# Optimization experiments

Measured on AMD Instinct MI355X. Metric: run time of the kernel, lower is better.

Reference implementation:

```python
import jax, jax.numpy as jnp
import numpy as np

B, L, D, H, NL, C = 8, 512, 64, 256, 2, 8
EPS = 1e-5
NEG = -1e9


def _causal_softmax(scores):
    # scores: (B, L, L); lower-triangular causal mask then softmax over last dim
    Ls = scores.shape[-1]
    mask = jnp.tril(jnp.ones((Ls, Ls), dtype=bool))
    return jax.nn.softmax(jnp.where(mask, scores, NEG), axis=-1)


def _attn_plain(x):
    s = jnp.einsum('bld,bmd->blm', x, x)
    return jnp.einsum('blm,bmd->bld', _causal_softmax(s), x)


def _attn_sdpa(x):
    s = jnp.einsum('bld,bmd->blm', x, x) / jnp.sqrt(jnp.float32(x.shape[-1]))
    return jnp.einsum('blm,bmd->bld', _causal_softmax(s), x)


def _attn_additive(x):
    # materializes (B, L, L, D) as in the original module
    s = jnp.tanh(x[:, :, None, :] + x[:, None, :, :]).sum(axis=-1)  # (B,L,L)
    return jnp.einsum('blm,bmd->bld', _causal_softmax(s), x)


def _bn(x, gamma, beta):
    # training-mode BatchNorm1d over (B, L) per feature; x: (B, L, F)
    mu = x.mean(axis=(0, 1))
    var = ((x - mu) ** 2).mean(axis=(0, 1))
    return (x - mu) * jax.lax.rsqrt(var + EPS) * gamma + beta


def _lstm_layer(x, Wih, Whh, bih, bhh):
    # x: (B, L, K) -> (B, L, H). PyTorch gate order: i, f, g, o.
    Hh = Whh.shape[1]
    xg = jnp.einsum('blk,gk->blg', x, Wih) + bih + bhh  # (B, L, 4H)
    xg = jnp.swapaxes(xg, 0, 1)  # (L, B, 4H)

    def step(carry, xt):
        h, c = carry
        g = xt + h @ Whh.T
        i = jax.nn.sigmoid(g[:, 0 * Hh:1 * Hh])
        f = jax.nn.sigmoid(g[:, 1 * Hh:2 * Hh])
        gg = jnp.tanh(g[:, 2 * Hh:3 * Hh])
        o = jax.nn.sigmoid(g[:, 3 * Hh:4 * Hh])
        c = f * c + i * gg
        h = o * jnp.tanh(c)
        return (h, c), h

    h0 = jnp.zeros((x.shape[0], Hh), x.dtype)
    _, hs = jax.lax.scan(step, (h0, h0), xg)
    return jnp.swapaxes(hs, 0, 1)  # (B, L, H)


def setup_inputs() -> dict:
    key = jax.random.key(0)
    ks = jax.random.split(key, 20)
    s = 1.0 / np.sqrt(H)
    u = lambda k, sh: jax.random.uniform(k, sh, jnp.float32, -s, s)
    return {
        'src': jax.random.normal(ks[0], (B, L, D), jnp.float32),
        'attn_w': jax.random.uniform(ks[1], (3, L, D), jnp.float32, 0.5, 1.5),
        'cat_w': jax.random.uniform(ks[2], (3, L, H), jnp.float32, 0.5, 1.5),
        'bn1_gamma': 1.0 + 0.1 * jax.random.normal(ks[3], (3, D), jnp.float32),
        'bn1_beta': 0.1 * jax.random.normal(ks[4], (3, D), jnp.float32),
        'bn2_gamma': 1.0 + 0.1 * jax.random.normal(ks[5], (H,), jnp.float32),
        'bn2_beta': 0.1 * jax.random.normal(ks[6], (H,), jnp.float32),
        'Wih0': u(ks[7], (3, 4 * H, D)),
        'Whh0': u(ks[8], (3, 4 * H, H)),
        'bih0': u(ks[9], (3, 4 * H)),
        'bhh0': u(ks[10], (3, 4 * H)),
        'Wih1': u(ks[11], (3, 4 * H, H)),
        'Whh1': u(ks[12], (3, 4 * H, H)),
        'bih1': u(ks[13], (3, 4 * H)),
        'bhh1': u(ks[14], (3, 4 * H)),
        'fc_W': u(ks[15], (C, H)),
        'fc_b': u(ks[16], (C,)),
    }


def reference(src, attn_w, cat_w, bn1_gamma, bn1_beta, bn2_gamma, bn2_beta,
              Wih0, Whh0, bih0, bhh0, Wih1, Whh1, bih1, bhh1, fc_W, fc_b):
    # three attentions, normalized weighted sum
    outs = jnp.stack([_attn_plain(src), _attn_additive(src), _attn_sdpa(src)])  # (3,B,L,D)
    aw = attn_w / attn_w.sum(axis=0)  # (3, L, D)
    attention_output = jnp.einsum('kbld,kld->bld', outs, aw)

    line1 = _bn(src, bn1_gamma[0], bn1_beta[0])
    line2 = _bn(src + attention_output, bn1_gamma[1], bn1_beta[1])
    line3 = _bn(attention_output, bn1_gamma[2], bn1_beta[2])

    def lstm2(x, i):
        h = _lstm_layer(x, Wih0[i], Whh0[i], bih0[i], bhh0[i])
        return _lstm_layer(h, Wih1[i], Whh1[i], bih1[i], bhh1[i])

    l1 = lstm2(line1, 0)
    l2 = lstm2(line2, 1)
    l3 = lstm2(line3, 2)

    cw = cat_w / cat_w.sum(axis=0)  # (3, L, H)
    cat = l1 * cw[0] + l2 * cw[1] + l3 * cw[2]
    cat = _bn(cat, bn2_gamma, bn2_beta)
    # eval-mode dropout is identity
    return cat[:, -1, :] @ fc_W.T + fc_b  # (B, C)
```

## Files before the change

### kernel.cpp

```cpp
#include <hip/hip_runtime.h>

#define B_ 8
#define L_ 512
#define D_ 64
#define H_ 256
#define GH 1024
#define EPS_ 1e-5f
#define POISON_ 0xAAAAAAAAu

typedef float f32x4 __attribute__((ext_vector_type(4)));
typedef _Float16 half8 __attribute__((ext_vector_type(8)));

__device__ __forceinline__ unsigned short f2h(float f) {
  _Float16 h = (_Float16)f;
  return __builtin_bit_cast(unsigned short, h);
}
__device__ __forceinline__ float h2f(unsigned short s) {
  _Float16 h = __builtin_bit_cast(_Float16, s);
  return (float)h;
}
__device__ __forceinline__ float fast_tanh(float x) {
  return 1.0f - 2.0f / (1.0f + __expf(2.0f * x));
}
__device__ __forceinline__ float fast_sig(float x) {
  return 1.0f / (1.0f + __expf(-x));
}
__device__ __forceinline__ unsigned int load_agent(const unsigned int* p) {
  return __hip_atomic_load(p, __ATOMIC_RELAXED, __HIP_MEMORY_SCOPE_AGENT);
}

__global__ void scores_kernel(const float* __restrict__ src,
                              float* __restrict__ Sp, float* __restrict__ Sa) {
  const int l = blockIdx.x, b = blockIdx.y;
  __shared__ float xl[D_];
  if (threadIdx.x < D_) xl[threadIdx.x] = src[(b * L_ + l) * D_ + threadIdx.x];
  __syncthreads();
  for (int m = threadIdx.x; m <= l; m += blockDim.x) {
    const float4* xr = (const float4*)&src[(b * L_ + m) * D_];
    float dp = 0.f, da = 0.f;
#pragma unroll
    for (int d4 = 0; d4 < D_ / 4; ++d4) {
      float4 v = xr[d4];
      dp += xl[d4*4+0]*v.x + xl[d4*4+1]*v.y + xl[d4*4+2]*v.z + xl[d4*4+3]*v.w;
      da += fast_tanh(xl[d4*4+0]+v.x) + fast_tanh(xl[d4*4+1]+v.y)
          + fast_tanh(xl[d4*4+2]+v.z) + fast_tanh(xl[d4*4+3]+v.w);
    }
    Sp[(b * L_ + l) * L_ + m] = dp;
    Sa[(b * L_ + l) * L_ + m] = da;
  }
}

__global__ void softmax_av_kernel(const float* __restrict__ src, const float* __restrict__ Sp,
                                  const float* __restrict__ Sa, float* __restrict__ outk) {
  const int l = blockIdx.x, b = blockIdx.y, k = blockIdx.z;
  const int lane = threadIdx.x;
  __shared__ float p[L_];
  const float* row = (k == 1) ? &Sa[(b * L_ + l) * L_] : &Sp[(b * L_ + l) * L_];
  const float scale = (k == 2) ? 0.125f : 1.0f;
  float mx = -1e30f;
  for (int m = lane; m <= l; m += 64) { float v = row[m] * scale; p[m] = v; mx = fmaxf(mx, v); }
#pragma unroll
  for (int off = 32; off > 0; off >>= 1) mx = fmaxf(mx, __shfl_xor(mx, off, 64));
  float sum = 0.f;
  for (int m = lane; m <= l; m += 64) { float e = __expf(p[m] - mx); p[m] = e; sum += e; }
#pragma unroll
  for (int off = 32; off > 0; off >>= 1) sum += __shfl_xor(sum, off, 64);
  __syncthreads();
  const float inv = 1.0f / sum;
  float acc = 0.f;
  for (int m = 0; m <= l; ++m) acc += p[m] * src[(b * L_ + m) * D_ + lane];
  outk[((k * B_ + b) * L_ + l) * D_ + lane] = acc * inv;
}

__global__ void combine_kernel(const float* __restrict__ outk, const float* __restrict__ attn_w,
                               float* __restrict__ attn) {
  int i = blockIdx.x * blockDim.x + threadIdx.x;
  if (i >= B_ * L_ * D_) return;
  int ld = i & (L_ * D_ - 1);
  float w0 = attn_w[ld], w1 = attn_w[L_ * D_ + ld], w2 = attn_w[2 * L_ * D_ + ld];
  float o0 = outk[i], o1 = outk[B_ * L_ * D_ + i], o2 = outk[2 * B_ * L_ * D_ + i];
  attn[i] = (o0 * w0 + o1 * w1 + o2 * w2) / (w0 + w1 + w2);
}

__global__ void bn1_kernel(const float* __restrict__ src, const float* __restrict__ attn,
                           const float* __restrict__ gamma, const float* __restrict__ beta,
                           float* __restrict__ line_in) {
  const int d = blockIdx.x, line = blockIdx.y;
  float s1 = 0.f, s2 = 0.f;
  for (int i = threadIdx.x; i < B_ * L_; i += blockDim.x) {
    float v = (line == 0) ? src[i * D_ + d]
            : (line == 1) ? src[i * D_ + d] + attn[i * D_ + d]
                          : attn[i * D_ + d];
    s1 += v; s2 += v * v;
  }
#pragma unroll
  for (int off = 32; off > 0; off >>= 1) { s1 += __shfl_xor(s1, off, 64); s2 += __shfl_xor(s2, off, 64); }
  __shared__ float a1[4], a2[4];
  __shared__ float mean_s, rstd_s;
  int w = threadIdx.x >> 6;
  if ((threadIdx.x & 63) == 0) { a1[w] = s1; a2[w] = s2; }
  __syncthreads();
  if (threadIdx.x == 0) {
    float t1 = a1[0] + a1[1] + a1[2] + a1[3];
    float t2 = a2[0] + a2[1] + a2[2] + a2[3];
    float mean = t1 / (float)(B_ * L_);
    float var = t2 / (float)(B_ * L_) - mean * mean;
    mean_s = mean; rstd_s = rsqrtf(var + EPS_);
  }
  __syncthreads();
  const float mean = mean_s;
  const float gs = gamma[line * D_ + d] * rstd_s, be = beta[line * D_ + d];
  for (int i = threadIdx.x; i < B_ * L_; i += blockDim.x) {
    float v = (line == 0) ? src[i * D_ + d]
            : (line == 1) ? src[i * D_ + d] + attn[i * D_ + d]
                          : attn[i * D_ + d];
    line_in[line * B_ * L_ * D_ + i * D_ + d] = (v - mean) * gs + be;
  }
}

template <int IN_K>
__device__ __forceinline__ void rec_body(
    const float* __restrict__ in_f32,
    const unsigned short* __restrict__ in_b16,
    const float* __restrict__ Wih, const float* __restrict__ Whh,
    const float* __restrict__ bih, const float* __restrict__ bhh,
    unsigned short* __restrict__ hseq,
    int line, int s,
    unsigned short* hprev, unsigned short* inbuf,
    float (*gbuf)[32][8], float (*biasS)[32]) {
  constexpr int INROW = IN_K + 8;
  constexpr int NKT_IN = IN_K / 32;
  const int tid = threadIdx.x, w = tid >> 6, lane = tid & 63;
  const int q = lane >> 4, col = lane & 15;

  half8 whhF[2][8];
  half8 wihF[2][NKT_IN];
#pragma unroll
  for (int T = 0; T < 2; ++T) {
    const int n = w * H_ + s * 32 + T * 16 + col;
    const float* wr = &Whh[(line * GH + n) * H_];
#pragma unroll
    for (int kt = 0; kt < 8; ++kt) {
      const float* pk = wr + kt * 32 + q * 8;
      half8 t;
#pragma unroll
      for (int j = 0; j < 8; ++j) t[j] = (_Float16)pk[j];
      whhF[T][kt] = t;
    }
    const float* wr2 = &Wih[(line * GH + n) * IN_K];
#pragma unroll
    for (int kt = 0; kt < NKT_IN; ++kt) {
      const float* pk = wr2 + kt * 32 + q * 8;
      half8 t;
#pragma unroll
      for (int j = 0; j < 8; ++j) t[j] = (_Float16)pk[j];
      wihF[T][kt] = t;
    }
  }
  if (tid < 128) {
    int g = tid >> 5, j = tid & 31;
    int n = g * H_ + s * 32 + j;
    biasS[g][j] = bih[line * GH + n] + bhh[line * GH + n];
  }
  for (int i = tid; i < 16 * 264; i += 256) hprev[i] = 0;
  for (int i = tid; i < 16 * INROW; i += 256) inbuf[i] = 0;

  int gdst[4];
  bool gremote[4];
  int goff[4];
#pragma unroll
  for (int rr = 0; rr < 4; ++rr) {
    int u = tid + rr * 256;
    int r = u >> 7, v = u & 127, b = v >> 4, pz = v & 15;
    int cidx = r * 32 + pz * 2;
    gremote[rr] = (r != s);
    gdst[rr] = b * 264 + cidx;
    goff[rr] = b * H_ + cidx;
  }

  if constexpr (IN_K == 64) {
#pragma unroll
    for (int r = 0; r < 2; ++r) {
      int idx = tid + r * 256;
      int b = idx >> 6, d = idx & 63;
      inbuf[b * INROW + d] = f2h(in_f32[(line * B_ * L_ + b * L_ + 0) * D_ + d]);
    }
  } else {
    const unsigned int* sa[4];
    unsigned int sv[4];
#pragma unroll
    for (int r = 0; r < 4; ++r) {
      int u = tid + r * 256;
      int b = u >> 7, pr = u & 127;
      sa[r] = (const unsigned int*)&in_b16[((line * L_ + 0) * B_ + b) * H_ + pr * 2];
    }
    bool ready = false;
    while (!ready) {
#pragma unroll
      for (int r = 0; r < 4; ++r) sv[r] = load_agent(sa[r]);
      ready = true;
#pragma unroll
      for (int r = 0; r < 4; ++r) ready = ready && (sv[r] != POISON_);
    }
#pragma unroll
    for (int r = 0; r < 4; ++r) {
      int u = tid + r * 256;
      int b = u >> 7, pr = u & 127;
      *(unsigned int*)&inbuf[b * INROW + pr * 2] = sv[r];
    }
  }

  float c0 = 0.f, c1 = 0.f;
  const int ub = tid & 7, jp = (tid >> 3) * 2;
  __syncthreads();

  for (int t = 0; t < L_; ++t) {
    f32x4 acc0 = {0.f, 0.f, 0.f, 0.f}, acc1 = {0.f, 0.f, 0.f, 0.f};
#pragma unroll
    for (int kt = 0; kt < NKT_IN; ++kt) {
      half8 a = *(const half8*)&inbuf[col * INROW + kt * 32 + q * 8];
      acc0 = __builtin_amdgcn_mfma_f32_16x16x32_f16(a, wihF[0][kt], acc0, 0, 0, 0);
      acc1 = __builtin_amdgcn_mfma_f32_16x16x32_f16(a, wihF[1][kt], acc1, 0, 0, 0);
    }
#pragma unroll
    for (int kt = 0; kt < 8; ++kt) {
      half8 a = *(const half8*)&hprev[col * 264 + kt * 32 + q * 8];
      acc0 = __builtin_amdgcn_mfma_f32_16x16x32_f16(a, whhF[0][kt], acc0, 0, 0, 0);
      acc1 = __builtin_amdgcn_mfma_f32_16x16x32_f16(a, whhF[1][kt], acc1, 0, 0, 0);
    }
    if (q < 2) {
#pragma unroll
      for (int r = 0; r < 4; ++r) {
        gbuf[w][col][q * 4 + r] = acc0[r];
        gbuf[w][16 + col][q * 4 + r] = acc1[r];
      }
    }
    __syncthreads();

    if (tid < 128) {
      float gi0 = gbuf[0][jp][ub] + biasS[0][jp];
      float gf0 = gbuf[1][jp][ub] + biasS[1][jp];
      float gg0 = gbuf[2][jp][ub] + biasS[2][jp];
      float go0 = gbuf[3][jp][ub] + biasS[3][jp];
      float gi1 = gbuf[0][jp+1][ub] + biasS[0][jp+1];
      float gf1 = gbuf[1][jp+1][ub] + biasS[1][jp+1];
      float gg1 = gbuf[2][jp+1][ub] + biasS[2][jp+1];
      float go1 = gbuf[3][jp+1][ub] + biasS[3][jp+1];
      c0 = fast_sig(gf0) * c0 + fast_sig(gi0) * fast_tanh(gg0);
      c1 = fast_sig(gf1) * c1 + fast_sig(gi1) * fast_tanh(gg1);
      float h0 = fast_sig(go0) * fast_tanh(c0);
      float h1 = fast_sig(go1) * fast_tanh(c1);
      unsigned int packed = (unsigned int)f2h(h0) | ((unsigned int)f2h(h1) << 16);
      if (packed == POISON_) packed ^= 1u;
      __hip_atomic_store(
          (unsigned int*)&hseq[((line * L_ + t) * B_ + ub) * H_ + s * 32 + jp],
          packed, __ATOMIC_RELAXED, __HIP_MEMORY_SCOPE_AGENT);
      *(unsigned int*)&hprev[ub * 264 + s * 32 + jp] = packed;
    }

    if (t == L_ - 1) break;

    const unsigned short* hrow = &hseq[(size_t)(line * L_ + t) * B_ * H_];
    const unsigned int* ga[4];
    unsigned int gv[4];
#pragma unroll
    for (int rr = 0; rr < 4; ++rr) ga[rr] = (const unsigned int*)(hrow + goff[rr]);

    if constexpr (IN_K == 64) {
#pragma unroll
      for (int r = 0; r < 2; ++r) {
        int idx = tid + r * 256;
        int b = idx >> 6, d = idx & 63;
        inbuf[b * INROW + d] = f2h(in_f32[(line * B_ * L_ + b * L_ + t + 1) * D_ + d]);
      }
      bool ready = false;
      while (!ready) {
#pragma unroll
        for (int rr = 0; rr < 4; ++rr) gv[rr] = load_agent(ga[rr]);
        ready = true;
#pragma unroll
        for (int rr = 0; rr < 4; ++rr)
          ready = ready && (!gremote[rr] || gv[rr] != POISON_);
      }
    } else {
      const unsigned int* sa[4];
      unsigned int sv[4];
#pragma unroll
      for (int r = 0; r < 4; ++r) {
        int u = tid + r * 256;
        int b = u >> 7, pr = u & 127;
        sa[r] = (const unsigned int*)&in_b16[((line * L_ + t + 1) * B_ + b) * H_ + pr * 2];
      }
      bool ready = false;
      while (!ready) {
#pragma unroll
        for (int rr = 0; rr < 4; ++rr) gv[rr] = load_agent(ga[rr]);
#pragma unroll
        for (int r = 0; r < 4; ++r) sv[r] = load_agent(sa[r]);
        ready = true;
#pragma unroll
        for (int rr = 0; rr < 4; ++rr)
          ready = ready && (!gremote[rr] || gv[rr] != POISON_);
#pragma unroll
        for (int r = 0; r < 4; ++r) ready = ready && (sv[r] != POISON_);
      }
#pragma unroll
      for (int r = 0; r < 4; ++r) {
        int u = tid + r * 256;
        int b = u >> 7, pr = u & 127;
        *(unsigned int*)&inbuf[b * INROW + pr * 2] = sv[r];
      }
    }
#pragma unroll
    for (int rr = 0; rr < 4; ++rr)
      if (gremote[rr]) *(unsigned int*)&hprev[gdst[rr]] = gv[rr];
    __syncthreads();
  }
}

__global__ __launch_bounds__(256, 1) void rec_fused_kernel(
    const float* __restrict__ line_in,
    const float* __restrict__ Wih0, const float* __restrict__ Whh0,
    const float* __restrict__ bih0, const float* __restrict__ bhh0,
    const float* __restrict__ Wih1, const float* __restrict__ Whh1,
    const float* __restrict__ bih1, const float* __restrict__ bhh1,
    unsigned short* __restrict__ hseq0, unsigned short* __restrict__ hseq1) {
  __shared__ unsigned short hprev[16 * 264];
  __shared__ unsigned short inbuf[16 * 264];
  __shared__ float gbuf[4][32][8];
  __shared__ float biasS[4][32];
  const int blk = blockIdx.x;
  const int layer = blk / 24, rem = blk % 24;
  const int line = rem >> 3, s = rem & 7;
  if (layer == 0)
    rec_body<64>(line_in, nullptr, Wih0, Whh0, bih0, bhh0, hseq0,
                 line, s, hprev, inbuf, gbuf, biasS);
  else
    rec_body<256>(nullptr, hseq0, Wih1, Whh1, bih1, bhh1, hseq1,
                  line, s, hprev, inbuf, gbuf, biasS);
}

__global__ void bn2stats_kernel(const unsigned short* __restrict__ hseq1,
                                const float* __restrict__ cat_w, float* __restrict__ stats) {
  const int h = blockIdx.x;
  float s1 = 0.f, s2 = 0.f;
  for (int i = threadIdx.x; i < B_ * L_; i += blockDim.x) {
    int l = i >> 3, b = i & 7;
    float w0 = cat_w[(0 * L_ + l) * H_ + h], w1 = cat_w[(1 * L_ + l) * H_ + h],
          w2 = cat_w[(2 * L_ + l) * H_ + h];
    float v0 = h2f(hseq1[((0 * L_ + l) * B_ + b) * H_ + h]);
    float v1 = h2f(hseq1[((1 * L_ + l) * B_ + b) * H_ + h]);
    float v2 = h2f(hseq1[((2 * L_ + l) * B_ + b) * H_ + h]);
    float v = (v0 * w0 + v1 * w1 + v2 * w2) / (w0 + w1 + w2);
    s1 += v; s2 += v * v;
  }
#pragma unroll
  for (int off = 32; off > 0; off >>= 1) { s1 += __shfl_xor(s1, off, 64); s2 += __shfl_xor(s2, off, 64); }
  __shared__ float a1[4], a2[4];
  int w = threadIdx.x >> 6;
  if ((threadIdx.x & 63) == 0) { a1[w] = s1; a2[w] = s2; }
  __syncthreads();
  if (threadIdx.x == 0) {
    float t1 = a1[0] + a1[1] + a1[2] + a1[3];
    float t2 = a2[0] + a2[1] + a2[2] + a2[3];
    float mean = t1 / (float)(B_ * L_);
    float var = t2 / (float)(B_ * L_) - mean * mean;
    stats[2 * h] = mean;
    stats[2 * h + 1] = rsqrtf(var + EPS_);
  }
}

__global__ void final_kernel(const unsigned short* __restrict__ hseq1,
                             const float* __restrict__ cat_w, const float* __restrict__ stats,
                             const float* __restrict__ gamma, const float* __restrict__ beta,
                             const float* __restrict__ fcW, const float* __restrict__ fcb,
                             float* __restrict__ out) {
  const int h = threadIdx.x;
  __shared__ float vmat[B_][H_];
  const float mean = stats[2 * h], rstd = stats[2 * h + 1];
  const float g = gamma[h], be = beta[h];
  const int l = L_ - 1;
  float w0 = cat_w[(0 * L_ + l) * H_ + h], w1 = cat_w[(1 * L_ + l) * H_ + h],
        w2 = cat_w[(2 * L_ + l) * H_ + h];
  const float wsum = w0 + w1 + w2;
  for (int b = 0; b < B_; ++b) {
    float v0 = h2f(hseq1[((0 * L_ + l) * B_ + b) * H_ + h]);
    float v1 = h2f(hseq1[((1 * L_ + l) * B_ + b) * H_ + h]);
    float v2 = h2f(hseq1[((2 * L_ + l) * B_ + b) * H_ + h]);
    float v = (v0 * w0 + v1 * w1 + v2 * w2) / wsum;
    vmat[b][h] = (v - mean) * rstd * g + be;
  }
  __syncthreads();
  if (h < 64) {
    int b = h >> 3, c = h & 7;
    float acc = fcb[c];
    for (int k = 0; k < H_; ++k) acc += vmat[b][k] * fcW[c * H_ + k];
    out[b * 8 + c] = acc;
  }
}

extern "C" void kernel_launch(void* const* d_in, const int* in_sizes, int n_in,
                              void* d_out, int out_size, void* d_ws, size_t ws_size,
                              hipStream_t stream) {
  (void)in_sizes; (void)n_in; (void)out_size; (void)ws_size;
  const float* src       = (const float*)d_in[0];
  const float* attn_w    = (const float*)d_in[1];
  const float* cat_w     = (const float*)d_in[2];
  const float* bn1_gamma = (const float*)d_in[3];
  const float* bn1_beta  = (const float*)d_in[4];
  const float* bn2_gamma = (const float*)d_in[5];
  const float* bn2_beta  = (const float*)d_in[6];
  const float* Wih0      = (const float*)d_in[7];
  const float* Whh0      = (const float*)d_in[8];
  const float* bih0      = (const float*)d_in[9];
  const float* bhh0      = (const float*)d_in[10];
  const float* Wih1      = (const float*)d_in[11];
  const float* Whh1      = (const float*)d_in[12];
  const float* bih1      = (const float*)d_in[13];
  const float* bhh1      = (const float*)d_in[14];
  const float* fcW       = (const float*)d_in[15];
  const float* fcb       = (const float*)d_in[16];
  float* out = (float*)d_out;

  char* p = (char*)d_ws;
  float* Sp = (float*)p;                      p += (size_t)B_ * L_ * L_ * 4;
  float* Sa = (float*)p;                      p += (size_t)B_ * L_ * L_ * 4;
  float* outk = (float*)p;                    p += (size_t)3 * B_ * L_ * D_ * 4;
  float* attn = (float*)p;                    p += (size_t)B_ * L_ * D_ * 4;
  float* line_in = (float*)p;                 p += (size_t)3 * B_ * L_ * D_ * 4;
  float* stats = (float*)p;                   p += (size_t)512 * 4;
  unsigned short* hseq0 = (unsigned short*)p; p += (size_t)3 * L_ * B_ * H_ * 2;
  unsigned short* hseq1 = (unsigned short*)p; p += (size_t)3 * L_ * B_ * H_ * 2;

  scores_kernel<<<dim3(L_, B_), dim3(256), 0, stream>>>(src, Sp, Sa);
  softmax_av_kernel<<<dim3(L_, B_, 3), dim3(64), 0, stream>>>(src, Sp, Sa, outk);
  combine_kernel<<<dim3((B_ * L_ * D_) / 256), dim3(256), 0, stream>>>(outk, attn_w, attn);
  bn1_kernel<<<dim3(D_, 3), dim3(256), 0, stream>>>(src, attn, bn1_gamma, bn1_beta, line_in);
  rec_fused_kernel<<<dim3(48), dim3(256), 0, stream>>>(
      line_in, Wih0, Whh0, bih0, bhh0, Wih1, Whh1, bih1, bhh1, hseq0, hseq1);
  bn2stats_kernel<<<dim3(H_), dim3(256), 0, stream>>>(hseq1, cat_w, stats);
  final_kernel<<<dim3(1), dim3(256), 0, stream>>>(hseq1, cat_w, stats, bn2_gamma, bn2_beta,
                                                  fcW, fcb, out);
}
```

Before: 1.300 ms.

## Restructure LSTM: one block per recurrence, precompute input projections in separate GEMMs

Replaces the 8-block-per-line recurrence, which exchanged hidden-state slices through global memory every step, with a single 512-thread block per line and layer that keeps the full Whh in registers and LDS. The input projections move out of the serial loop: layer 0's into a separate xg0 kernel, layer 1's into concurrent GEMM blocks that consume hseq0 in chunks through poison-flag polling. This targets per-step cross-block synchronisation latency and the input-projection work on the critical path. The cost is extra workspace for the fp16 xg buffers, a large dynamic LDS allocation, and reliance on all 18 blocks being co-resident for the flag-based producer/consumer handoff.

```diff
diff --git a/kernel.cpp b/kernel.cpp
--- a/kernel.cpp
+++ b/kernel.cpp
@@ -10,6 +10,9 @@
 
 typedef float f32x4 __attribute__((ext_vector_type(4)));
 typedef _Float16 half8 __attribute__((ext_vector_type(8)));
+typedef unsigned long long u64_;
+
+#define MFMA16(a, b, c) __builtin_amdgcn_mfma_f32_16x16x32_f16((a), (b), (c), 0, 0, 0)
 
 __device__ __forceinline__ unsigned short f2h(float f) {
   _Float16 h = (_Float16)f;
@@ -25,8 +28,18 @@
 __device__ __forceinline__ float fast_sig(float x) {
   return 1.0f / (1.0f + __expf(-x));
 }
-__device__ __forceinline__ unsigned int load_agent(const unsigned int* p) {
-  return __hip_atomic_load(p, __ATOMIC_RELAXED, __HIP_MEMORY_SCOPE_AGENT);
+__device__ __forceinline__ unsigned int pack2h(float x, float y) {
+  return (unsigned int)f2h(x) | ((unsigned int)f2h(y) << 16);
+}
+__device__ __forceinline__ unsigned int fixp(unsigned int d) { return d == POISON_ ? (d ^ 1u) : d; }
+__device__ __forceinline__ u64_ fixp64(u64_ v) {
+  return (u64_)fixp((unsigned int)v) | ((u64_)fixp((unsigned int)(v >> 32)) << 32);
+}
+__device__ __forceinline__ u64_ ldA64(const void* p) {
+  return __hip_atomic_load((const u64_*)p, __ATOMIC_RELAXED, __HIP_MEMORY_SCOPE_AGENT);
+}
+__device__ __forceinline__ void stA64(void* p, u64_ v) {
+  __hip_atomic_store((u64_*)p, v, __ATOMIC_RELAXED, __HIP_MEMORY_SCOPE_AGENT);
 }
 
 __global__ void scores_kernel(const float* __restrict__ src,
@@ -118,226 +131,263 @@
   }
 }
 
-template <int IN_K>
-__device__ __forceinline__ void rec_body(
-    const float* __restrict__ in_f32,
-    const unsigned short* __restrict__ in_b16,
-    const float* __restrict__ Wih, const float* __restrict__ Whh,
-    const float* __restrict__ bih, const float* __restrict__ bhh,
-    unsigned short* __restrict__ hseq,
-    int line, int s,
-    unsigned short* hprev, unsigned short* inbuf,
-    float (*gbuf)[32][8], float (*biasS)[32]) {
-  constexpr int INROW = IN_K + 8;
-  constexpr int NKT_IN = IN_K / 32;
-  const int tid = threadIdx.x, w = tid >> 6, lane = tid & 63;
-  const int q = lane >> 4, col = lane & 15;
-
-  half8 whhF[2][8];
-  half8 wihF[2][NKT_IN];
-#pragma unroll
-  for (int T = 0; T < 2; ++T) {
-    const int n = w * H_ + s * 32 + T * 16 + col;
-    const float* wr = &Whh[(line * GH + n) * H_];
-#pragma unroll
-    for (int kt = 0; kt < 8; ++kt) {
-      const float* pk = wr + kt * 32 + q * 8;
-      half8 t;
-#pragma unroll
-      for (int j = 0; j < 8; ++j) t[j] = (_Float16)pk[j];
-      whhF[T][kt] = t;
-    }
-    const float* wr2 = &Wih[(line * GH + n) * IN_K];
-#pragma unroll
-    for (int kt = 0; kt < NKT_IN; ++kt) {
-      const float* pk = wr2 + kt * 32 + q * 8;
-      half8 t;
-#pragma unroll
-      for (int j = 0; j < 8; ++j) t[j] = (_Float16)pk[j];
-      wihF[T][kt] = t;
-    }
-  }
-  if (tid < 128) {
-    int g = tid >> 5, j = tid & 31;
-    int n = g * H_ + s * 32 + j;
-    biasS[g][j] = bih[line * GH + n] + bhh[line * GH + n];
-  }
-  for (int i = tid; i < 16 * 264; i += 256) hprev[i] = 0;
-  for (int i = tid; i < 16 * INROW; i += 256) inbuf[i] = 0;
-
-  int gdst[4];
-  bool gremote[4];
-  int goff[4];
-#pragma unroll
-  for (int rr = 0; rr < 4; ++rr) {
-    int u = tid + rr * 256;
-    int r = u >> 7, v = u & 127, b = v >> 4, pz = v & 15;
-    int cidx = r * 32 + pz * 2;
-    gremote[rr] = (r != s);
-    gdst[rr] = b * 264 + cidx;
-    goff[rr] = b * H_ + cidx;
-  }
-
-  if constexpr (IN_K == 64) {
-#pragma unroll
-    for (int r = 0; r < 2; ++r) {
-      int idx = tid + r * 256;
-      int b = idx >> 6, d = idx & 63;
-      inbuf[b * INROW + d] = f2h(in_f32[(line * B_ * L_ + b * L_ + 0) * D_ + d]);
-    }
+__global__ __launch_bounds__(512) void xg0_kernel(
+    const float* __restrict__ line_in, const float* __restrict__ Wih0,
+    const float* __restrict__ bih0, const float* __restrict__ bhh0,
+    unsigned short* __restrict__ xg0) {
+  __shared__ unsigned short af[256][72];
+  const int tc = blockIdx.x, line = blockIdx.y;
+  const int tid = threadIdx.x;
+  for (int idx = tid; idx < 4096; idx += 512) {
+    int row = idx >> 4, d4 = (idx & 15) * 4;
+    int t = tc * 32 + (row >> 3), b = row & 7;
+    float4 v = *(const float4*)&line_in[(size_t)line * (B_ * L_ * D_) + ((size_t)b * L_ + t) * D_ + d4];
+    u64_ pk = (u64_)f2h(v.x) | ((u64_)f2h(v.y) << 16) | ((u64_)f2h(v.z) << 32) | ((u64_)f2h(v.w) << 48);
+    *(u64_*)&af[row][d4] = pk;
+  }
+  __syncthreads();
+  const int lane = tid & 63, w = tid >> 6, col = lane & 15, q = lane >> 4;
+  unsigned short* xg_l = xg0 + (size_t)line * 4194304;
+#pragma unroll 1
+  for (int nt = w; nt < 64; nt += 8) {
+    const int n = nt * 16 + col;
+    const float* wr = &Wih0[((size_t)line * GH + n) * D_ + q * 8];
+    half8 b0, b1;
+    {
+      float4 u0 = *(const float4*)wr, u1 = *(const float4*)(wr + 4);
+      float4 u2 = *(const float4*)(wr + 32), u3 = *(const float4*)(wr + 36);
+      b0[0] = (_Float16)u0.x; b0[1] = (_Float16)u0.y; b0[2] = (_Float16)u0.z; b0[3] = (_Float16)u0.w;
+      b0[4] = (_Float16)u1.x; b0[5] = (_Float16)u1.y; b0[6] = (_Float16)u1.z; b0[7] = (_Float16)u1.w;
+      b1[0] = (_Float16)u2.x; b1[1] = (_Float16)u2.y; b1[2] = (_Float16)u2.z; b1[3] = (_Float16)u2.w;
+      b1[4] = (_Float16)u3.x; b1[5] = (_Float16)u3.y; b1[6] = (_Float16)u3.z; b1[7] = (_Float16)u3.w;
+    }
+    const float bias = bih0[line * GH + n] + bhh0[line * GH + n];
+#pragma unroll 1
+    for (int mt = 0; mt < 16; ++mt) {
+      f32x4 acc = {0.f, 0.f, 0.f, 0.f};
+      half8 av0 = *(const half8*)&af[mt * 16 + col][q * 8];
+      half8 av1 = *(const half8*)&af[mt * 16 + col][32 + q * 8];
+      acc = MFMA16(av0, b0, acc);
+      acc = MFMA16(av1, b1, acc);
+      unsigned int d0 = fixp(pack2h(acc[0] + bias, acc[1] + bias));
+      unsigned int d1 = fixp(pack2h(acc[2] + bias, acc[3] + bias));
+      int t = tc * 32 + mt * 2 + (q >> 1);
+      *(u64_*)&xg_l[(size_t)t * 8192 + n * 8 + (q & 1) * 4] = (u64_)d0 | ((u64_)d1 << 32);
+    }
+  }
+}
+
+__device__ __forceinline__ void rec_core(
+    const float* __restrict__ Whh_l, const unsigned short* __restrict__ xg_l,
+    unsigned short* __restrict__ hseq_l, unsigned short* sm) {
+  unsigned short* wlds = sm;
+  unsigned short* hb = sm + 65536;
+  const int tid = threadIdx.x, lane = tid & 63, w = tid >> 6;
+  const int col = lane & 15, q = lane >> 4, qq = q & 1;
+
+  for (int idx = tid; idx < 8192; idx += 512) {
+    int rec = idx >> 6, l = idx & 63;
+    int ww = rec >> 4, tau = (rec >> 1) & 7, ktp = rec & 1;
+    int n = (tau >> 1) * 256 + ww * 32 + (tau & 1) * 16 + (l & 15);
+    const float* p = &Whh_l[(size_t)n * H_ + 192 + ktp * 32 + (l >> 4) * 8];
+    float4 u0 = *(const float4*)p, u1 = *(const float4*)(p + 4);
+    half8 tf;
+    tf[0] = (_Float16)u0.x; tf[1] = (_Float16)u0.y; tf[2] = (_Float16)u0.z; tf[3] = (_Float16)u0.w;
+    tf[4] = (_Float16)u1.x; tf[5] = (_Float16)u1.y; tf[6] = (_Float16)u1.z; tf[7] = (_Float16)u1.w;
+    *(half8*)&wlds[(size_t)idx * 8] = tf;
+  }
+
+  half8 wf[6][8];
+#pragma unroll
+  for (int g = 0; g < 4; ++g)
+#pragma unroll
+    for (int h2 = 0; h2 < 2; ++h2) {
+      const float* wr = &Whh_l[(size_t)(g * 256 + w * 32 + h2 * 16 + col) * H_];
+#pragma unroll
+      for (int kt = 0; kt < 6; ++kt) {
+        const float* p = wr + kt * 32 + q * 8;
+        float4 u0 = *(const float4*)p, u1 = *(const float4*)(p + 4);
+        half8 tf;
+        tf[0] = (_Float16)u0.x; tf[1] = (_Float16)u0.y; tf[2] = (_Float16)u0.z; tf[3] = (_Float16)u0.w;
+        tf[4] = (_Float16)u1.x; tf[5] = (_Float16)u1.y; tf[6] = (_Float16)u1.z; tf[7] = (_Float16)u1.w;
+        wf[kt][g * 2 + h2] = tf;
+      }
+    }
+
+  for (int i = tid; i < 8448; i += 512) hb[i] = 0;
+  float c_[2][4] = {{0.f, 0.f, 0.f, 0.f}, {0.f, 0.f, 0.f, 0.f}};
+  __syncthreads();
+
+  int cur = 0;
+#pragma unroll 1
+  for (int t = 0; t < L_; ++t) {
+    const unsigned short* hbr = hb + cur * 4224;
+    unsigned short* hbw = hb + (cur ^ 1) * 4224;
+
+    if (t > 0) {
+      u64_ v = fixp64(*(const u64_*)&hbr[w * 264 + lane * 4]);
+      stA64(&hseq_l[((size_t)(t - 1) * 8 + w) * 256 + lane * 4], v);
+    }
+
+#pragma unroll
+    for (int h2 = 0; h2 < 2; ++h2) {
+      u64_ xv[4];
+      const size_t xb = (size_t)t * 8192 + (size_t)qq * 4;
+#pragma unroll
+      for (int g = 0; g < 4; ++g)
+        xv[g] = ldA64(&xg_l[xb + (unsigned)(g * 2048 + w * 256 + h2 * 128 + col * 8)]);
+
+      f32x4 a0 = {0.f, 0.f, 0.f, 0.f}, a1 = a0, a2 = a0, a3 = a0;
+#pragma unroll
+      for (int kt = 0; kt < 6; ++kt) {
+        half8 av = *(const half8*)&hbr[col * 264 + kt * 32 + q * 8];
+        a0 = MFMA16(av, wf[kt][0 + h2], a0);
+        a1 = MFMA16(av, wf[kt][2 + h2], a1);
+        a2 = MFMA16(av, wf[kt][4 + h2], a2);
+        a3 = MFMA16(av, wf[kt][6 + h2], a3);
+      }
+#pragma unroll
+      for (int ktp = 0; ktp < 2; ++ktp) {
+        half8 av = *(const half8*)&hbr[col * 264 + 192 + ktp * 32 + q * 8];
+        half8 b0 = *(const half8*)&wlds[((w * 16 + (0 + h2) * 2 + ktp) * 64 + lane) * 8];
+        half8 b1 = *(const half8*)&wlds[((w * 16 + (2 + h2) * 2 + ktp) * 64 + lane) * 8];
+        half8 b2 = *(const half8*)&wlds[((w * 16 + (4 + h2) * 2 + ktp) * 64 + lane) * 8];
+        half8 b3 = *(const half8*)&wlds[((w * 16 + (6 + h2) * 2 + ktp) * 64 + lane) * 8];
+        a0 = MFMA16(av, b0, a0); a1 = MFMA16(av, b1, a1);
+        a2 = MFMA16(av, b2, a2); a3 = MFMA16(av, b3, a3);
+      }
+
+      for (;;) {
+        bool bad = false;
+#pragma unroll
+        for (int g = 0; g < 4; ++g)
+          bad = bad | ((unsigned int)xv[g] == POISON_) | ((unsigned int)(xv[g] >> 32) == POISON_);
+        if (!bad) break;
+#pragma unroll
+        for (int g = 0; g < 4; ++g)
+          xv[g] = ldA64(&xg_l[xb + (unsigned)(g * 2048 + w * 256 + h2 * 128 + col * 8)]);
+      }
+
+      if (lane < 32) {
+#pragma unroll
+        for (int rr = 0; rr < 4; ++rr) {
+          float gi = a0[rr] + h2f((unsigned short)(xv[0] >> (16 * rr)));
+          float gf = a1[rr] + h2f((unsigned short)(xv[1] >> (16 * rr)));
+          float gg = a2[rr] + h2f((unsigned short)(xv[2] >> (16 * rr)));
+          float go = a3[rr] + h2f((unsigned short)(xv[3] >> (16 * rr)));
+          float cv = fast_sig(gf) * c_[h2][rr] + fast_sig(gi) * fast_tanh(gg);
+          c_[h2][rr] = cv;
+          float hv = fast_sig(go) * fast_tanh(cv);
+          hbw[(q * 4 + rr) * 264 + w * 32 + h2 * 16 + col] = f2h(hv);
+        }
+      }
+    }
+    __syncthreads();
+    cur ^= 1;
+  }
+  {
+    const unsigned short* hbr = hb + cur * 4224;
+    u64_ v = fixp64(*(const u64_*)&hbr[w * 264 + lane * 4]);
+    stA64(&hseq_l[((size_t)(L_ - 1) * 8 + w) * 256 + lane * 4], v);
+  }
+}
+
+__device__ __forceinline__ void gemm1_core(
+    const unsigned short* __restrict__ hs0_l, const float* __restrict__ Wih_l,
+    const float* __restrict__ bih_l, const float* __restrict__ bhh_l,
+    unsigned short* __restrict__ xg_l, int nq, unsigned short* sm) {
+  unsigned short* wlds = sm;
+  unsigned short* as_ = sm + 65536;
+  const int tid = threadIdx.x, lane = tid & 63, w = tid >> 6;
+  const int col = lane & 15, q = lane >> 4;
+
+  for (int idx = tid; idx < 8192; idx += 512) {
+    int rec = idx >> 6, l = idx & 63;
+    int nt = rec >> 3, kt = rec & 7;
+    int n = nq * 256 + nt * 16 + (l & 15);
+    const float* p = &Wih_l[(size_t)n * H_ + kt * 32 + (l >> 4) * 8];
+    float4 u0 = *(const float4*)p, u1 = *(const float4*)(p + 4);
+    half8 tf;
+    tf[0] = (_Float16)u0.x; tf[1] = (_Float16)u0.y; tf[2] = (_Float16)u0.z; tf[3] = (_Float16)u0.w;
+    tf[4] = (_Float16)u1.x; tf[5] = (_Float16)u1.y; tf[6] = (_Float16)u1.z; tf[7] = (_Float16)u1.w;
+    *(half8*)&wlds[(size_t)idx * 8] = tf;
+  }
+  const int nA = nq * 256 + w * 16 + col, nB = nA + 128;
+  const float biasA = bih_l[nA] + bhh_l[nA];
+  const float biasB = bih_l[nB] + bhh_l[nB];
+  __syncthreads();
+
+#pragma unroll 1
+  for (int c = 0; c < 128; ++c) {
+    const u64_* src = (const u64_*)&hs0_l[(size_t)c * 8192] + tid * 4;
+    u64_ v0, v1, v2, v3;
+    for (;;) {
+      v0 = ldA64(src + 0); v1 = ldA64(src + 1); v2 = ldA64(src + 2); v3 = ldA64(src + 3);
+      bool bad = ((unsigned int)v0 == POISON_) | ((unsigned int)(v0 >> 32) == POISON_)
+               | ((unsigned int)v1 == POISON_) | ((unsigned int)(v1 >> 32) == POISON_)
+               | ((unsigned int)v2 == POISON_) | ((unsigned int)(v2 >> 32) == POISON_)
+               | ((unsigned int)v3 == POISON_) | ((unsigned int)(v3 >> 32) == POISON_);
+      if (!bad) break;
+    }
+    __syncthreads();
+    {
+      u64_* d = (u64_*)&as_[(tid >> 4) * 264 + (tid & 15) * 16];
+      d[0] = v0; d[1] = v1; d[2] = v2; d[3] = v3;
+    }
+    __syncthreads();
+
+    half8 afr[2][8];
+#pragma unroll
+    for (int mt = 0; mt < 2; ++mt)
+#pragma unroll
+      for (int kt = 0; kt < 8; ++kt)
+        afr[mt][kt] = *(const half8*)&as_[(mt * 16 + col) * 264 + kt * 32 + q * 8];
+
+    const int t0 = c * 4;
+#pragma unroll
+    for (int half = 0; half < 2; ++half) {
+      const int nt = w + half * 8;
+      const float bias = half ? biasB : biasA;
+      f32x4 c0 = {0.f, 0.f, 0.f, 0.f}, c1 = c0;
+#pragma unroll
+      for (int kt = 0; kt < 8; ++kt) {
+        half8 bf = *(const half8*)&wlds[((nt * 8 + kt) * 64 + lane) * 8];
+        c0 = MFMA16(afr[0][kt], bf, c0);
+        c1 = MFMA16(afr[1][kt], bf, c1);
+      }
+      const int n = nq * 256 + nt * 16 + col;
+#pragma unroll
+      for (int mt = 0; mt < 2; ++mt) {
+        const f32x4 A = mt ? c1 : c0;
+        unsigned int d0 = fixp(pack2h(A[0] + bias, A[1] + bias));
+        unsigned int d1 = fixp(pack2h(A[2] + bias, A[3] + bias));
+        int t = t0 + mt * 2 + (q >> 1);
+        stA64(&xg_l[(size_t)t * 8192 + n * 8 + (q & 1) * 4], (u64_)d0 | ((u64_)d1 << 32));
+      }
+    }
+  }
+}
+
+__global__ __launch_bounds__(512, 2) void rec2_kernel(
+    const float* __restrict__ Whh0, const float* __restrict__ Whh1,
+    const float* __restrict__ Wih1, const float* __restrict__ bih1,
+    const float* __restrict__ bhh1,
+    const unsigned short* __restrict__ xg0, unsigned short* __restrict__ xg1,
+    unsigned short* __restrict__ hseq0, unsigned short* __restrict__ hseq1) {
+  extern __shared__ unsigned short sm[];
+  const int blk = blockIdx.x;
+  if (blk < 6) {
+    const int line = blk % 3, layer = blk / 3;
+    const float* Whh_l = (layer ? Whh1 : Whh0) + (size_t)line * GH * H_;
+    const unsigned short* xg_l = (layer ? (const unsigned short*)xg1 : xg0) + (size_t)line * 4194304;
+    unsigned short* hs_l = (layer ? hseq1 : hseq0) + (size_t)line * (L_ * B_ * H_);
+    rec_core(Whh_l, xg_l, hs_l, sm);
   } else {
-    const unsigned int* sa[4];
-    unsigned int sv[4];
-#pragma unroll
-    for (int r = 0; r < 4; ++r) {
-      int u = tid + r * 256;
-      int b = u >> 7, pr = u & 127;
-      sa[r] = (const unsigned int*)&in_b16[((line * L_ + 0) * B_ + b) * H_ + pr * 2];
-    }
-    bool ready = false;
-    while (!ready) {
-#pragma unroll
-      for (int r = 0; r < 4; ++r) sv[r] = load_agent(sa[r]);
-      ready = true;
-#pragma unroll
-      for (int r = 0; r < 4; ++r) ready = ready && (sv[r] != POISON_);
-    }
-#pragma unroll
-    for (int r = 0; r < 4; ++r) {
-      int u = tid + r * 256;
-      int b = u >> 7, pr = u & 127;
-      *(unsigned int*)&inbuf[b * INROW + pr * 2] = sv[r];
-    }
-  }
-
-  float c0 = 0.f, c1 = 0.f;
-  const int ub = tid & 7, jp = (tid >> 3) * 2;
-  __syncthreads();
-
-  for (int t = 0; t < L_; ++t) {
-    f32x4 acc0 = {0.f, 0.f, 0.f, 0.f}, acc1 = {0.f, 0.f, 0.f, 0.f};
-#pragma unroll
-    for (int kt = 0; kt < NKT_IN; ++kt) {
-      half8 a = *(const half8*)&inbuf[col * INROW + kt * 32 + q * 8];
-      acc0 = __builtin_amdgcn_mfma_f32_16x16x32_f16(a, wihF[0][kt], acc0, 0, 0, 0);
-      acc1 = __builtin_amdgcn_mfma_f32_16x16x32_f16(a, wihF[1][kt], acc1, 0, 0, 0);
-    }
-#pragma unroll
-    for (int kt = 0; kt < 8; ++kt) {
-      half8 a = *(const half8*)&hprev[col * 264 + kt * 32 + q * 8];
-      acc0 = __builtin_amdgcn_mfma_f32_16x16x32_f16(a, whhF[0][kt], acc0, 0, 0, 0);
-      acc1 = __builtin_amdgcn_mfma_f32_16x16x32_f16(a, whhF[1][kt], acc1, 0, 0, 0);
-    }
-    if (q < 2) {
-#pragma unroll
-      for (int r = 0; r < 4; ++r) {
-        gbuf[w][col][q * 4 + r] = acc0[r];
-        gbuf[w][16 + col][q * 4 + r] = acc1[r];
-      }
-    }
-    __syncthreads();
-
-    if (tid < 128) {
-      float gi0 = gbuf[0][jp][ub] + biasS[0][jp];
-      float gf0 = gbuf[1][jp][ub] + biasS[1][jp];
-      float gg0 = gbuf[2][jp][ub] + biasS[2][jp];
-      float go0 = gbuf[3][jp][ub] + biasS[3][jp];
-      float gi1 = gbuf[0][jp+1][ub] + biasS[0][jp+1];
-      float gf1 = gbuf[1][jp+1][ub] + biasS[1][jp+1];
-      float gg1 = gbuf[2][jp+1][ub] + biasS[2][jp+1];
-      float go1 = gbuf[3][jp+1][ub] + biasS[3][jp+1];
-      c0 = fast_sig(gf0) * c0 + fast_sig(gi0) * fast_tanh(gg0);
-      c1 = fast_sig(gf1) * c1 + fast_sig(gi1) * fast_tanh(gg1);
-      float h0 = fast_sig(go0) * fast_tanh(c0);
-      float h1 = fast_sig(go1) * fast_tanh(c1);
-      unsigned int packed = (unsigned int)f2h(h0) | ((unsigned int)f2h(h1) << 16);
-      if (packed == POISON_) packed ^= 1u;
-      __hip_atomic_store(
-          (unsigned int*)&hseq[((line * L_ + t) * B_ + ub) * H_ + s * 32 + jp],
-          packed, __ATOMIC_RELAXED, __HIP_MEMORY_SCOPE_AGENT);
-      *(unsigned int*)&hprev[ub * 264 + s * 32 + jp] = packed;
-    }
-
-    if (t == L_ - 1) break;
-
-    const unsigned short* hrow = &hseq[(size_t)(line * L_ + t) * B_ * H_];
-    const unsigned int* ga[4];
-    unsigned int gv[4];
-#pragma unroll
-    for (int rr = 0; rr < 4; ++rr) ga[rr] = (const unsigned int*)(hrow + goff[rr]);
-
-    if constexpr (IN_K == 64) {
-#pragma unroll
-      for (int r = 0; r < 2; ++r) {
-        int idx = tid + r * 256;
-        int b = idx >> 6, d = idx & 63;
-        inbuf[b * INROW + d] = f2h(in_f32[(line * B_ * L_ + b * L_ + t + 1) * D_ + d]);
-      }
-      bool ready = false;
-      while (!ready) {
-#pragma unroll
-        for (int rr = 0; rr < 4; ++rr) gv[rr] = load_agent(ga[rr]);
-        ready = true;
-#pragma unroll
-        for (int rr = 0; rr < 4; ++rr)
-          ready = ready && (!gremote[rr] || gv[rr] != POISON_);
-      }
-    } else {
-      const unsigned int* sa[4];
-      unsigned int sv[4];
-#pragma unroll
-      for (int r = 0; r < 4; ++r) {
-        int u = tid + r * 256;
-        int b = u >> 7, pr = u & 127;
-        sa[r] = (const unsigned int*)&in_b16[((line * L_ + t + 1) * B_ + b) * H_ + pr * 2];
-      }
-      bool ready = false;
-      while (!ready) {
-#pragma unroll
-        for (int rr = 0; rr < 4; ++rr) gv[rr] = load_agent(ga[rr]);
-#pragma unroll
-        for (int r = 0; r < 4; ++r) sv[r] = load_agent(sa[r]);
-        ready = true;
-#pragma unroll
-        for (int rr = 0; rr < 4; ++rr)
-          ready = ready && (!gremote[rr] || gv[rr] != POISON_);
-#pragma unroll
-        for (int r = 0; r < 4; ++r) ready = ready && (sv[r] != POISON_);
-      }
-#pragma unroll
-      for (int r = 0; r < 4; ++r) {
-        int u = tid + r * 256;
-        int b = u >> 7, pr = u & 127;
-        *(unsigned int*)&inbuf[b * INROW + pr * 2] = sv[r];
-      }
-    }
-#pragma unroll
-    for (int rr = 0; rr < 4; ++rr)
-      if (gremote[rr]) *(unsigned int*)&hprev[gdst[rr]] = gv[rr];
-    __syncthreads();
-  }
-}
-
-__global__ __launch_bounds__(256, 1) void rec_fused_kernel(
-    const float* __restrict__ line_in,
-    const float* __restrict__ Wih0, const float* __restrict__ Whh0,
-    const float* __restrict__ bih0, const float* __restrict__ bhh0,
-    const float* __restrict__ Wih1, const float* __restrict__ Whh1,
-    const float* __restrict__ bih1, const float* __restrict__ bhh1,
-    unsigned short* __restrict__ hseq0, unsigned short* __restrict__ hseq1) {
-  __shared__ unsigned short hprev[16 * 264];
-  __shared__ unsigned short inbuf[16 * 264];
-  __shared__ float gbuf[4][32][8];
-  __shared__ float biasS[4][32];
-  const int blk = blockIdx.x;
-  const int layer = blk / 24, rem = blk % 24;
-  const int line = rem >> 3, s = rem & 7;
-  if (layer == 0)
-    rec_body<64>(line_in, nullptr, Wih0, Whh0, bih0, bhh0, hseq0,
-                 line, s, hprev, inbuf, gbuf, biasS);
-  else
-    rec_body<256>(nullptr, hseq0, Wih1, Whh1, bih1, bhh1, hseq1,
-                  line, s, hprev, inbuf, gbuf, biasS);
+    const int g = blk - 6, line = g % 3, nq = g / 3;
+    gemm1_core(hseq0 + (size_t)line * (L_ * B_ * H_), Wih1 + (size_t)line * GH * H_,
+               bih1 + (size_t)line * GH, bhh1 + (size_t)line * GH,
+               xg1 + (size_t)line * 4194304, nq, sm);
+  }
 }
 
 __global__ void bn2stats_kernel(const unsigned short* __restrict__ hseq1,
@@ -431,13 +481,16 @@
   float* stats = (float*)p;                   p += (size_t)512 * 4;
   unsigned short* hseq0 = (unsigned short*)p; p += (size_t)3 * L_ * B_ * H_ * 2;
   unsigned short* hseq1 = (unsigned short*)p; p += (size_t)3 * L_ * B_ * H_ * 2;
+  unsigned short* xg0 = (unsigned short*)p;   p += (size_t)3 * L_ * GH * B_ * 2;
+  unsigned short* xg1 = (unsigned short*)p;   p += (size_t)3 * L_ * GH * B_ * 2;
 
   scores_kernel<<<dim3(L_, B_), dim3(256), 0, stream>>>(src, Sp, Sa);
   softmax_av_kernel<<<dim3(L_, B_, 3), dim3(64), 0, stream>>>(src, Sp, Sa, outk);
   combine_kernel<<<dim3((B_ * L_ * D_) / 256), dim3(256), 0, stream>>>(outk, attn_w, attn);
   bn1_kernel<<<dim3(D_, 3), dim3(256), 0, stream>>>(src, attn, bn1_gamma, bn1_beta, line_in);
-  rec_fused_kernel<<<dim3(48), dim3(256), 0, stream>>>(
-      line_in, Wih0, Whh0, bih0, bhh0, Wih1, Whh1, bih1, bhh1, hseq0, hseq1);
+  xg0_kernel<<<dim3(16, 3), dim3(512), 0, stream>>>(line_in, Wih0, bih0, bhh0, xg0);
+  rec2_kernel<<<dim3(18), dim3(512), 147968, stream>>>(
+      Whh0, Whh1, Wih1, bih1, bhh1, xg0, xg1, hseq0, hseq1);
   bn2stats_kernel<<<dim3(H_), dim3(256), 0, stream>>>(hseq1, cat_w, stats);
   final_kernel<<<dim3(1), dim3(256), 0, stream>>>(hseq1, cat_w, stats, bn2_gamma, bn2_beta,
                                                   fcW, fcb, out);
```

Result: slower. 3.650 ms (+180.7%).
